# Kernel optimization log

Hardware: AMD Instinct MI355X
Metric: run time of the kernel (lower is better)

## Reference

```python
import jax, jax.numpy as jnp
import numpy as np

RADIUS = 0.4
NSAMPLE = 32
NORMALIZE_DP = True


def setup_inputs() -> dict:
    key = jax.random.key(0)
    k1, k2, k3 = jax.random.split(key, 3)
    B, N, K, C = 2, 16384, 4096, 128
    xyz = jax.random.normal(k1, (B, N, 3), dtype=jnp.float32)
    new_xyz = jax.random.normal(k2, (B, K, 3), dtype=jnp.float32)
    features = jax.random.normal(k3, (B, C, N), dtype=jnp.float32)
    return {"xyz": xyz, "new_xyz": new_xyz, "features": features}


def _ball_query(radius, nsample, xyz, new_xyz):
    # xyz: (B,N,3), new_xyz: (B,K,3) -> indices (B,K,nsample) int32
    N = xyz.shape[1]
    # squared distances via ||a||^2 + ||b||^2 - 2 a.b  -> (B,K,N)
    d2 = (jnp.sum(new_xyz * new_xyz, -1)[:, :, None]
          + jnp.sum(xyz * xyz, -1)[:, None, :]
          - 2.0 * jnp.einsum('bkd,bnd->bkn', new_xyz, xyz))
    mask = d2 < radius * radius
    # key = point index if inside ball else N (sentinel); take nsample smallest
    key = jnp.where(mask, jnp.arange(N, dtype=jnp.int32), jnp.int32(N))
    neg_top, _ = jax.lax.top_k(-key, nsample)  # (B,K,nsample)
    idx = -neg_top
    # pointnet2 semantics: pad with first in-radius index (0 if ball empty)
    first = idx[..., :1]
    first = jnp.where(first < N, first, 0)
    idx = jnp.where(idx < N, idx, first)
    return idx


def _group(features, idx):
    # features: (B,C,N), idx: (B,K,ns) -> (B,C,K,ns)
    return jax.vmap(lambda f, i: f[:, i])(features, idx)


def reference(xyz, new_xyz, features):
    idx = _ball_query(RADIUS, NSAMPLE, xyz, new_xyz)          # (B,K,ns)
    xyz_t = jnp.transpose(xyz, (0, 2, 1))                      # (B,3,N)
    grouped_xyz = _group(xyz_t, idx)                           # (B,3,K,ns)
    grouped_xyz = grouped_xyz - jnp.transpose(new_xyz, (0, 2, 1))[..., None]
    if NORMALIZE_DP:
        grouped_xyz = grouped_xyz / RADIUS
    grouped_features = _group(features, idx)                   # (B,C,K,ns)
    return (grouped_xyz, grouped_features)
```

## Files before the change

### kernel.cpp

```cpp
#include <hip/hip_runtime.h>

#define BB 2
#define NN 16384
#define KK 4096
#define CC 128
#define SS 32

typedef float vfloat4 __attribute__((ext_vector_type(4)));

__global__ __launch_bounds__(256) void transpose_prep_kernel(
    const float* __restrict__ feat, const float* __restrict__ xyz,
    float* __restrict__ feat_t, float* __restrict__ xyzw)
{
    __shared__ float tile[64][133];
    const int b  = blockIdx.x >> 8;
    const int n0 = (blockIdx.x & 255) * 64;
    const int t  = threadIdx.x;

    if (t < 64) {
        const int i = b * NN + n0 + t;
        const float* p = xyz + (size_t)i * 3;
        const float x = p[0], y = p[1], z = p[2];
        const float pp = __fadd_rn(__fadd_rn(__fmul_rn(x, x), __fmul_rn(y, y)),
                                   __fmul_rn(z, z));
        vfloat4 v = {x, y, z, pp};
        *(vfloat4*)(xyzw + (size_t)i * 4) = v;
    }

    const int ln = t & 63;
    const int cr = t >> 6;
#pragma unroll
    for (int p = 0; p < 32; ++p) {
        const int c = p * 4 + cr;
        tile[ln][c] = feat[((size_t)b * CC + c) * NN + n0 + ln];
    }
    __syncthreads();

    const int cl = t & 31;
    const int ns = t >> 5;
#pragma unroll
    for (int p = 0; p < 8; ++p) {
        const int n = ns + 8 * p;
        float* dst = feat_t + ((size_t)(b * NN + n0 + n)) * CC;
#pragma unroll
        for (int j = 0; j < 4; ++j)
            dst[cl + 32 * j] = tile[n][cl + 32 * j];
    }
}

__global__ __launch_bounds__(256) void ball_query_kernel(
    const float* __restrict__ xyzw,
    const float* __restrict__ new_xyz,
    int* __restrict__ idx_buf)
{
    const int wave = threadIdx.x >> 6;
    const int lane = threadIdx.x & 63;
    const int qi   = blockIdx.x * 4 + wave;
    const int b    = qi >> 12;
    const int k    = qi & (KK - 1);

    const float R2 = (float)(0.4 * 0.4);

    const float* q = new_xyz + (size_t)(b * KK + k) * 3;
    const float qx = q[0], qy = q[1], qz = q[2];
    const float qq = __fadd_rn(__fadd_rn(__fmul_rn(qx, qx), __fmul_rn(qy, qy)),
                               __fmul_rn(qz, qz));

    const vfloat4* xw = (const vfloat4*)xyzw + (size_t)b * NN;
    int* out = idx_buf + (size_t)qi * SS;

    int cnt = 0;
    int first = -1;

    auto process = [&](int base, vfloat4 v) {
        const float dot = __fadd_rn(__fadd_rn(__fmul_rn(qx, v.x), __fmul_rn(qy, v.y)),
                                    __fmul_rn(qz, v.z));
        const float d2 = __fsub_rn(__fadd_rn(qq, v.w), __fmul_rn(2.0f, dot));
        const bool inball = d2 < R2;
        const unsigned long long mask = __ballot(inball);
        if (mask) {
            if (first < 0) first = base + (int)__builtin_ctzll(mask);
            if (inball) {
                const int pos = cnt + __popcll(mask & ((1ull << lane) - 1ull));
                if (pos < SS) out[pos] = base + lane;
            }
            cnt += __popcll(mask);
        }
    };

    vfloat4 v0 = xw[lane];
    vfloat4 v1 = xw[64 + lane];
    vfloat4 v2 = xw[128 + lane];
    vfloat4 v3 = xw[192 + lane];

    for (int base = 0; base < NN; base += 256) {
        const int nb = (base + 256 < NN) ? base + 256 : 0;
        vfloat4 u0 = xw[nb + lane];
        vfloat4 u1 = xw[nb + 64 + lane];
        vfloat4 u2 = xw[nb + 128 + lane];
        vfloat4 u3 = xw[nb + 192 + lane];

        process(base, v0);
        process(base + 64, v1);
        process(base + 128, v2);
        process(base + 192, v3);
        if (cnt >= SS) break;

        v0 = u0; v1 = u1; v2 = u2; v3 = u3;
    }

    const int fill = (first < 0) ? 0 : first;
    if (lane < SS && lane >= cnt) out[lane] = fill;
}

__global__ __launch_bounds__(256) void group_kernel(
    const float* __restrict__ xyzw,
    const float* __restrict__ new_xyz,
    const float* __restrict__ feat_t,
    const int*   __restrict__ idx_buf,
    float* __restrict__ out)
{
    __shared__ float tile[SS * CC];
    __shared__ float txyz[3][SS];

    const int t    = threadIdx.x;
    const int l    = t & 63;
    const int w    = t >> 6;
    const int bk   = blockIdx.x;
    const int b    = bk >> 12;
    const int k    = bk & (KK - 1);
    const int half = l >> 5;
    const int cl   = l & 31;

#pragma unroll
    for (int p = 0; p < 4; ++p) {
        const int r = 8 * w + 2 * p;
        const int s = r + half;
        const int n = idx_buf[bk * SS + s];
        const int chunk = cl ^ ((s >> 2) & 7);
        const float* src = feat_t + ((size_t)(b * NN + n)) * CC + 4 * chunk;
        __builtin_amdgcn_global_load_lds(
            (const __attribute__((address_space(1))) void*)src,
            (__attribute__((address_space(3))) void*)(tile + r * CC),
            16, 0, 0);
    }

    if (t < SS) {
        const int n = idx_buf[bk * SS + t];
        const float* q = new_xyz + (size_t)bk * 3;
        const vfloat4 wv = *((const vfloat4*)xyzw + (size_t)b * NN + n);
        txyz[0][t] = (wv.x - q[0]) / 0.4f;
        txyz[1][t] = (wv.y - q[1]) / 0.4f;
        txyz[2][t] = (wv.z - q[2]) / 0.4f;
    }

    __syncthreads();

    float* out_xyz  = out;
    float* out_feat = out + (size_t)BB * 3 * KK * SS;

    const int sq = t & 7;
    const int c0 = t >> 3;
#pragma unroll
    for (int p = 0; p < 4; ++p) {
        const int c  = c0 + 32 * p;
        const int co = (((c >> 2) ^ sq) << 2) + (c & 3);
        vfloat4 v;
        v.x = tile[(4 * sq + 0) * CC + co];
        v.y = tile[(4 * sq + 1) * CC + co];
        v.z = tile[(4 * sq + 2) * CC + co];
        v.w = tile[(4 * sq + 3) * CC + co];
        __builtin_nontemporal_store(
            v, (vfloat4*)(out_feat + (((size_t)(b * CC + c) * KK + k) * SS + 4 * sq)));
    }

    if (t < 24) {
        const int d   = t >> 3;
        const int sq2 = t & 7;
        const vfloat4 v = *(vfloat4*)&txyz[d][4 * sq2];
        __builtin_nontemporal_store(
            v, (vfloat4*)(out_xyz + (((size_t)(b * 3 + d) * KK + k) * SS + 4 * sq2)));
    }
}

extern "C" void kernel_launch(void* const* d_in, const int* in_sizes, int n_in,
                              void* d_out, int out_size, void* d_ws, size_t ws_size,
                              hipStream_t stream) {
    const float* xyz     = (const float*)d_in[0];
    const float* new_xyz = (const float*)d_in[1];
    const float* feat    = (const float*)d_in[2];
    float* out = (float*)d_out;

    int*   idx_buf = (int*)d_ws;
    float* xyzw    = (float*)((char*)d_ws + (1 << 20));
    float* feat_t  = (float*)((char*)d_ws + (1 << 20) + (512 << 10));

    transpose_prep_kernel<<<dim3(BB * (NN / 64)), dim3(256), 0, stream>>>(
        feat, xyz, feat_t, xyzw);

    ball_query_kernel<<<dim3(BB * KK / 4), dim3(256), 0, stream>>>(
        xyzw, new_xyz, idx_buf);

    group_kernel<<<dim3(BB * KK), dim3(256), 0, stream>>>(
        xyzw, new_xyz, feat_t, idx_buf, out);
}
```

Baseline: 91.08 us.

## Split ball query into per-segment scans plus a prefix-sum merge

Replaces the one-wave-per-query ball query, which exits early, with a thread-per-query scan over 32 point segments. Each segment records up to 32 hits and a count. A merge kernel then prefix-sums the counts and gathers the first 32 indices in order. This trades early termination for more parallelism, so every query now tests all N points in full. It also uses the feature output buffer as scratch space for hits and counts, which is later overwritten.

```diff
diff --git a/kernel.cpp b/kernel.cpp
--- a/kernel.cpp
+++ b/kernel.cpp
@@ -5,6 +5,9 @@
 #define KK 4096
 #define CC 128
 #define SS 32
+#define SEG 32
+#define SEGN (NN / SEG)
+#define BKK (BB * KK)
 
 typedef float vfloat4 __attribute__((ext_vector_type(4)));
 
@@ -48,69 +51,83 @@
     }
 }
 
-__global__ __launch_bounds__(256) void ball_query_kernel(
+__global__ __launch_bounds__(256) void ball_seg_kernel(
     const float* __restrict__ xyzw,
     const float* __restrict__ new_xyz,
+    int* __restrict__ hits,
+    int* __restrict__ counts)
+{
+    const int t  = threadIdx.x;
+    const int qb = blockIdx.x;
+    const int s  = blockIdx.y;
+    const int qi = qb * 256 + t;
+    const int b  = qb >> 4;
+
+    const float R2 = (float)(0.4 * 0.4);
+
+    const float* q = new_xyz + (size_t)qi * 3;
+    const float qx = q[0], qy = q[1], qz = q[2];
+    const float qq = __fadd_rn(__fadd_rn(__fmul_rn(qx, qx), __fmul_rn(qy, qy)),
+                               __fmul_rn(qz, qz));
+
+    const vfloat4* xw = (const vfloat4*)xyzw + (size_t)b * NN;
+    int* hrow = hits + ((size_t)s * BKK + qi) * SS;
+
+    int cnt = 0;
+    const int n0 = s * SEGN;
+#pragma unroll 4
+    for (int i = 0; i < SEGN; ++i) {
+        const int n = n0 + i;
+        const vfloat4 P = xw[n];
+        const float dot = __fadd_rn(
+            __fadd_rn(__fmul_rn(qx, P.x), __fmul_rn(qy, P.y)),
+            __fmul_rn(qz, P.z));
+        const float d2 = __fsub_rn(__fadd_rn(qq, P.w), __fmul_rn(2.0f, dot));
+        if (d2 < R2 && cnt < SS) {
+            hrow[cnt] = n;
+            ++cnt;
+        }
+    }
+    counts[s * BKK + qi] = cnt;
+}
+
+__global__ __launch_bounds__(256) void merge_kernel(
+    const int* __restrict__ hits,
+    const int* __restrict__ counts,
     int* __restrict__ idx_buf)
 {
     const int wave = threadIdx.x >> 6;
     const int lane = threadIdx.x & 63;
     const int qi   = blockIdx.x * 4 + wave;
-    const int b    = qi >> 12;
-    const int k    = qi & (KK - 1);
-
-    const float R2 = (float)(0.4 * 0.4);
-
-    const float* q = new_xyz + (size_t)(b * KK + k) * 3;
-    const float qx = q[0], qy = q[1], qz = q[2];
-    const float qq = __fadd_rn(__fadd_rn(__fmul_rn(qx, qx), __fmul_rn(qy, qy)),
-                               __fmul_rn(qz, qz));
-
-    const vfloat4* xw = (const vfloat4*)xyzw + (size_t)b * NN;
-    int* out = idx_buf + (size_t)qi * SS;
-
-    int cnt = 0;
-    int first = -1;
-
-    auto process = [&](int base, vfloat4 v) {
-        const float dot = __fadd_rn(__fadd_rn(__fmul_rn(qx, v.x), __fmul_rn(qy, v.y)),
-                                    __fmul_rn(qz, v.z));
-        const float d2 = __fsub_rn(__fadd_rn(qq, v.w), __fmul_rn(2.0f, dot));
-        const bool inball = d2 < R2;
-        const unsigned long long mask = __ballot(inball);
-        if (mask) {
-            if (first < 0) first = base + (int)__builtin_ctzll(mask);
-            if (inball) {
-                const int pos = cnt + __popcll(mask & ((1ull << lane) - 1ull));
-                if (pos < SS) out[pos] = base + lane;
-            }
-            cnt += __popcll(mask);
-        }
-    };
-
-    vfloat4 v0 = xw[lane];
-    vfloat4 v1 = xw[64 + lane];
-    vfloat4 v2 = xw[128 + lane];
-    vfloat4 v3 = xw[192 + lane];
-
-    for (int base = 0; base < NN; base += 256) {
-        const int nb = (base + 256 < NN) ? base + 256 : 0;
-        vfloat4 u0 = xw[nb + lane];
-        vfloat4 u1 = xw[nb + 64 + lane];
-        vfloat4 u2 = xw[nb + 128 + lane];
-        vfloat4 u3 = xw[nb + 192 + lane];
-
-        process(base, v0);
-        process(base + 64, v1);
-        process(base + 128, v2);
-        process(base + 192, v3);
-        if (cnt >= SS) break;
-
-        v0 = u0; v1 = u1; v2 = u2; v3 = u3;
-    }
-
-    const int fill = (first < 0) ? 0 : first;
-    if (lane < SS && lane >= cnt) out[lane] = fill;
+
+    int c = (lane < SEG) ? counts[lane * BKK + qi] : 0;
+#pragma unroll
+    for (int d = 1; d < 64; d <<= 1) {
+        const int u = __shfl_up(c, d);
+        if (lane >= d) c += u;
+    }
+    const int total = __shfl(c, SEG - 1);
+
+    int lo = 0;
+#pragma unroll
+    for (int step = 16; step >= 1; step >>= 1) {
+        const int cand = lo + step;
+        const int pv = __shfl(c, cand - 1);
+        if (lane >= pv) lo = cand;
+    }
+    const int pex  = __shfl(c, (lo > 0) ? lo - 1 : 0);
+    const int excl = (lo > 0) ? pex : 0;
+    const int off  = lane - excl;
+
+    int v = 0;
+    if (lane < SS && lane < total)
+        v = hits[((size_t)lo * BKK + qi) * SS + off];
+
+    int first = __shfl(v, 0);
+    if (total == 0) first = 0;
+    const int outv = (lane < total) ? v : first;
+
+    if (lane < SS) idx_buf[(size_t)qi * SS + lane] = outv;
 }
 
 __global__ __launch_bounds__(256) void group_kernel(
@@ -195,12 +212,18 @@
     float* xyzw    = (float*)((char*)d_ws + (1 << 20));
     float* feat_t  = (float*)((char*)d_ws + (1 << 20) + (512 << 10));
 
+    int* hits   = (int*)(out + (size_t)BB * 3 * KK * SS);
+    int* counts = hits + (size_t)SEG * BKK * SS;
+
     transpose_prep_kernel<<<dim3(BB * (NN / 64)), dim3(256), 0, stream>>>(
         feat, xyz, feat_t, xyzw);
 
-    ball_query_kernel<<<dim3(BB * KK / 4), dim3(256), 0, stream>>>(
-        xyzw, new_xyz, idx_buf);
-
-    group_kernel<<<dim3(BB * KK), dim3(256), 0, stream>>>(
+    ball_seg_kernel<<<dim3(BKK / 256, SEG), dim3(256), 0, stream>>>(
+        xyzw, new_xyz, hits, counts);
+
+    merge_kernel<<<dim3(BKK / 4), dim3(256), 0, stream>>>(
+        hits, counts, idx_buf);
+
+    group_kernel<<<dim3(BKK), dim3(256), 0, stream>>>(
         xyzw, new_xyz, feat_t, idx_buf, out);
 }
```

New measurement: 118.6 us. 1.3x slower.

## Bucket-sort queries by radius so ball-query waves have similar early-exit cost

Applied to the files above, without the earlier changes.

Adds a single-block kernel that buckets the query points by squared norm using a shared histogram and prefix sum, writing a permutation map. The ball-query kernel then reads its query index through this map, so the four waves in a block, and blocks close together in launch order, scan similar numbers of points before reaching the early exit. This is meant to reduce load imbalance, since queries far from the origin scan much more of the point cloud. It costs an extra serial launch on one workgroup. The order inside each bucket depends on atomics and is nondeterministic, but each result is still written to its original slot.

```diff
diff --git a/kernel.cpp b/kernel.cpp
--- a/kernel.cpp
+++ b/kernel.cpp
@@ -5,6 +5,7 @@
 #define KK 4096
 #define CC 128
 #define SS 32
+#define BKK (BB * KK)
 
 typedef float vfloat4 __attribute__((ext_vector_type(4)));
 
@@ -48,14 +49,54 @@
     }
 }
 
+__global__ __launch_bounds__(1024) void qsort_kernel(
+    const float* __restrict__ new_xyz,
+    int* __restrict__ qmap)
+{
+    __shared__ int hist[64];
+    __shared__ int base[64];
+    __shared__ unsigned char bk[BKK];
+
+    const int t = threadIdx.x;
+    if (t < 64) hist[t] = 0;
+    __syncthreads();
+
+#pragma unroll
+    for (int c = 0; c < BKK / 1024; ++c) {
+        const int q = c * 1024 + t;
+        const float* p = new_xyz + (size_t)q * 3;
+        const float qq = p[0] * p[0] + p[1] * p[1] + p[2] * p[2];
+        int bkt = (int)(qq * 8.0f);
+        bkt = bkt > 63 ? 63 : bkt;
+        bk[q] = (unsigned char)bkt;
+        atomicAdd(&hist[bkt], 1);
+    }
+    __syncthreads();
+
+    if (t == 0) {
+        int s = 0;
+#pragma unroll
+        for (int i = 0; i < 64; ++i) { base[i] = s; s += hist[i]; }
+    }
+    __syncthreads();
+
+#pragma unroll
+    for (int c = 0; c < BKK / 1024; ++c) {
+        const int q = c * 1024 + t;
+        const int pos = atomicAdd(&base[bk[q]], 1);
+        qmap[pos] = q;
+    }
+}
+
 __global__ __launch_bounds__(256) void ball_query_kernel(
     const float* __restrict__ xyzw,
     const float* __restrict__ new_xyz,
+    const int* __restrict__ qmap,
     int* __restrict__ idx_buf)
 {
     const int wave = threadIdx.x >> 6;
     const int lane = threadIdx.x & 63;
-    const int qi   = blockIdx.x * 4 + wave;
+    const int qi   = qmap[blockIdx.x * 4 + wave];
     const int b    = qi >> 12;
     const int k    = qi & (KK - 1);
 
@@ -194,13 +235,16 @@
     int*   idx_buf = (int*)d_ws;
     float* xyzw    = (float*)((char*)d_ws + (1 << 20));
     float* feat_t  = (float*)((char*)d_ws + (1 << 20) + (512 << 10));
+    int*   qmap    = (int*)((char*)d_ws + (1 << 20) + (512 << 10) + (CC * NN * BB) * 4);
 
     transpose_prep_kernel<<<dim3(BB * (NN / 64)), dim3(256), 0, stream>>>(
         feat, xyz, feat_t, xyzw);
 
-    ball_query_kernel<<<dim3(BB * KK / 4), dim3(256), 0, stream>>>(
-        xyzw, new_xyz, idx_buf);
-
-    group_kernel<<<dim3(BB * KK), dim3(256), 0, stream>>>(
+    qsort_kernel<<<dim3(1), dim3(1024), 0, stream>>>(new_xyz, qmap);
+
+    ball_query_kernel<<<dim3(BKK / 4), dim3(256), 0, stream>>>(
+        xyzw, new_xyz, qmap, idx_buf);
+
+    group_kernel<<<dim3(BKK), dim3(256), 0, stream>>>(
         xyzw, new_xyz, feat_t, idx_buf, out);
 }
```

Measured after the change: 87.54 us. -3.9%, faster.
